# Performance work log

Measured on AMD Instinct MI355X. Metric: run time of the kernel, lower is better.

## Reference

```python
import jax, jax.numpy as jnp
import numpy as np
from jax import lax

EPS = 1e-05


def rmsnorm_axis1(x, w, eps=EPS):
    # RMS over channel axis (axis=1), scale by per-channel weight
    ms = jnp.mean(x * x, axis=1, keepdims=True)
    return x * lax.rsqrt(ms + eps) * w[None, :, None]


def dwconv1d(x, w, b, dilation):
    # x: [B, C, L]; w: [C, 1, K] depthwise (feature_group_count=C)
    pad = (w.shape[-1] - 1) // 2 * dilation
    y = lax.conv_general_dilated(
        x, w, window_strides=(1,), padding=[(pad, pad)],
        rhs_dilation=(dilation,), dimension_numbers=('NCH', 'OIH', 'NCH'),
        feature_group_count=x.shape[1])
    return y + b[None, :, None]


def setup_inputs() -> dict:
    key = jax.random.key(0)
    ks = jax.random.split(key, 12)
    B, C, L, K = 16, 512, 2048, 3
    s = 1.0 / np.sqrt(C)
    return {
        'number_log': jax.random.normal(ks[0], (B,), jnp.float32),
        'x': jax.random.normal(ks[1], (B, C, L), jnp.float32),
        'pre_w': jnp.ones((C,), jnp.float32),
        'conv_w': jax.random.normal(ks[2], (C, 1, K), jnp.float32) * 0.3,
        'conv_b': jnp.zeros((C,), jnp.float32),
        'conv1_w': jax.random.normal(ks[3], (C, 1, K), jnp.float32) * 0.3,
        'conv1_b': jnp.zeros((C,), jnp.float32),
        'conv2_w': jax.random.normal(ks[4], (C, 1, K), jnp.float32) * 0.3,
        'conv2_b': jnp.zeros((C,), jnp.float32),
        'gate_w': jax.random.normal(ks[5], (C, C), jnp.float32) * s,
        'gate_b': jnp.zeros((C,), jnp.float32),
        'post_w': jnp.ones((C,), jnp.float32),
        'logits_w': jax.random.normal(ks[6], (1, C, 1), jnp.float32) * s,
    }


def reference(number_log, x, pre_w, conv_w, conv_b, conv1_w, conv1_b,
              conv2_w, conv2_b, gate_w, gate_b, post_w, logits_w):
    # pre_norm over channel axis
    x_norm = rmsnorm_axis1(x, pre_w)
    # three dilated depthwise conv branches, summed
    x_d = (dwconv1d(x_norm, conv_w, conv_b, 1)
           + dwconv1d(x_norm, conv1_w, conv1_b, 2)
           + dwconv1d(x_norm, conv2_w, conv2_b, 4))
    # gate: Linear over channel dim of transposed input, SiLU
    gate = jax.nn.silu(jnp.einsum('bcl,dc->bdl', x_norm, gate_w)
                       + gate_b[None, :, None])
    x_d = rmsnorm_axis1(x_d * gate, post_w)
    # logits: 1x1 conv C->1, no bias
    out = jnp.einsum('bcl,oc->bol', x + x_d, logits_w[:, :, 0])
    return out
```

## Files before the change

kernel.cpp:

```cpp
#include <hip/hip_runtime.h>
#include <hip/hip_bf16.h>

#define BB 16
#define CC 512
#define LL 2048

typedef float f32x4 __attribute__((ext_vector_type(4)));
typedef short s16x8 __attribute__((ext_vector_type(8)));

static __device__ __forceinline__ float bf2f(unsigned short u) {
    union { unsigned int i; float f; } v; v.i = ((unsigned int)u) << 16; return v.f;
}
static __device__ __forceinline__ unsigned short f2bf(float f) {
    union { float fv; unsigned int i; } v; v.fv = f;
    unsigned int x = v.i;
    return (unsigned short)((x + 0x7FFFu + ((x >> 16) & 1u)) >> 16);
}

__global__ void k0_cast(const float* __restrict__ gw, unsigned short* __restrict__ gwb) {
    int i = blockIdx.x * 256 + threadIdx.x;
    if (i < CC * CC) gwb[i] = f2bf(gw[i]);
}

#define K1_ST 520
__global__ __launch_bounds__(256) void k1_rms_t(
    const float* __restrict__ x, const float* __restrict__ pre_w,
    unsigned short* __restrict__ xnt, float* __restrict__ invr) {
    __shared__ unsigned short tile[32 * K1_ST];
    __shared__ float red[32 * 33];
    __shared__ float pwS[CC];
    __shared__ float ivS[32];
    const int tid = threadIdx.x;
    const int b  = blockIdx.x >> 6;
    const int lt = blockIdx.x & 63;
    const int l0 = lt * 32;
    const float* xb = x + (size_t)(b * CC) * LL + l0;

    for (int i = tid; i < CC; i += 256) pwS[i] = pre_w[i];

    const int lq = tid & 7;
    const int cr = tid >> 3;
    f32x4 ssq = {0.f, 0.f, 0.f, 0.f};
    #pragma unroll
    for (int p = 0; p < 16; ++p) {
        int c = p * 32 + cr;
        f32x4 v = *(const f32x4*)(xb + (size_t)c * LL + lq * 4);
        #pragma unroll
        for (int r = 0; r < 4; ++r) {
            ssq[r] += v[r] * v[r];
            tile[(lq * 4 + r) * K1_ST + c] = f2bf(v[r]);
        }
    }
    #pragma unroll
    for (int r = 0; r < 4; ++r) red[(lq * 4 + r) * 33 + cr] = ssq[r];
    __syncthreads();
    if (tid < 32) {
        float s = 0.f;
        #pragma unroll
        for (int g = 0; g < 32; ++g) s += red[tid * 33 + g];
        float iv = rsqrtf(s * (1.0f / CC) + 1e-5f);
        ivS[tid] = iv;
        invr[b * LL + l0 + tid] = iv;
    }
    __syncthreads();
    unsigned short* xo = xnt + ((size_t)b * LL + l0) * CC;
    #pragma unroll
    for (int p = 0; p < 8; ++p) {
        int g = p * 256 + tid;
        int l = g >> 6, c8 = (g & 63) * 8;
        s16x8 t = *(const s16x8*)&tile[l * K1_ST + c8];
        f32x4 w0 = *(const f32x4*)&pwS[c8];
        f32x4 w1 = *(const f32x4*)&pwS[c8 + 4];
        float iv = ivS[l];
        s16x8 o;
        #pragma unroll
        for (int r = 0; r < 4; ++r) {
            o[r]     = (short)f2bf(bf2f((unsigned short)t[r])     * iv * w0[r]);
            o[r + 4] = (short)f2bf(bf2f((unsigned short)t[r + 4]) * iv * w1[r]);
        }
        *(s16x8*)(xo + (size_t)l * CC + c8) = o;
    }
}

__global__ __launch_bounds__(512, 2) void k2_gemm(
    const unsigned short* __restrict__ gwb,
    const unsigned short* __restrict__ xnt,
    const float* __restrict__ gate_b,
    unsigned short* __restrict__ gate) {
    __shared__ unsigned short As[2][256 * 64];
    __shared__ unsigned short Bs[2][256 * 64];
    const int tid = threadIdx.x;
    const int w = tid >> 6, lane = tid & 63;
    const int lo = lane & 15, hi = lane >> 4;
    const int wm = w >> 2, wn = w & 3;
    const int nt = blockIdx.x, mt = blockIdx.y, b = blockIdx.z;
    const int m0 = mt * 256, n0 = nt * 256;
    const unsigned short* Ab = gwb;
    const unsigned short* Bb = xnt + (size_t)b * LL * CC;

    #define K2_STG(pp, buf, kt_)                                                     \
        {                                                                            \
            int g = (pp) * 512 + tid;                                                \
            int row = g >> 3;                                                        \
            int ks = ((g & 7) * 8) ^ ((row & 4) ? 16 : 0);                           \
            __builtin_amdgcn_global_load_lds(                                        \
                (const __attribute__((address_space(1))) void*)(Ab + (size_t)(m0 + row) * CC + (kt_) * 64 + ks), \
                (__attribute__((address_space(3))) void*)(&As[buf][g * 8]),          \
                16, 0, 0);                                                           \
            __builtin_amdgcn_global_load_lds(                                        \
                (const __attribute__((address_space(1))) void*)(Bb + (size_t)(n0 + row) * CC + (kt_) * 64 + ks), \
                (__attribute__((address_space(3))) void*)(&Bs[buf][g * 8]),          \
                16, 0, 0);                                                           \
        }

    f32x4 acc[8][4] = {};

    #pragma unroll
    for (int p = 0; p < 4; ++p) K2_STG(p, 0, 0);
    asm volatile("s_waitcnt vmcnt(0)" ::: "memory");
    __builtin_amdgcn_s_barrier();

    #pragma unroll 2
    for (int kt = 0; kt < 8; ++kt) {
        const int cur = kt & 1;
        s16x8 bf[4][2];
        #pragma unroll
        for (int p = 0; p < 4; ++p) {
            s16x8 af[2][2];
            #pragma unroll
            for (int j = 0; j < 2; ++j) {
                int row = wm * 128 + (p * 2 + j) * 16 + lo;
                int kb = (row & 4) ? 16 : 0;
                #pragma unroll
                for (int kk = 0; kk < 2; ++kk)
                    af[j][kk] = *(const s16x8*)(&As[cur][row * 64 + ((kk * 32 + hi * 8) ^ kb)]);
            }
            if (p == 0) {
                #pragma unroll
                for (int ni = 0; ni < 4; ++ni) {
                    int row = wn * 64 + ni * 16 + lo;
                    int kb = (row & 4) ? 16 : 0;
                    #pragma unroll
                    for (int kk = 0; kk < 2; ++kk)
                        bf[ni][kk] = *(const s16x8*)(&Bs[cur][row * 64 + ((kk * 32 + hi * 8) ^ kb)]);
                }
            }
            if (kt < 7) K2_STG(p, cur ^ 1, kt + 1);
            __builtin_amdgcn_s_barrier();
            asm volatile("s_waitcnt lgkmcnt(0)" ::: "memory");
            __builtin_amdgcn_sched_barrier(0);
            __builtin_amdgcn_s_setprio(1);
            #pragma unroll
            for (int j = 0; j < 2; ++j)
                #pragma unroll
                for (int ni = 0; ni < 4; ++ni)
                    #pragma unroll
                    for (int kk = 0; kk < 2; ++kk)
                        acc[p * 2 + j][ni] = __builtin_amdgcn_mfma_f32_16x16x32_bf16(
                            af[j][kk], bf[ni][kk], acc[p * 2 + j][ni], 0, 0, 0);
            __builtin_amdgcn_s_setprio(0);
            if (p == 3) asm volatile("s_waitcnt vmcnt(0)" ::: "memory");
            __builtin_amdgcn_s_barrier();
        }
    }

    #pragma unroll
    for (int mi = 0; mi < 8; ++mi) {
        #pragma unroll
        for (int ni = 0; ni < 4; ++ni) {
            int n = n0 + wn * 64 + ni * 16 + lo;
            int d0 = m0 + wm * 128 + mi * 16 + hi * 4;
            #pragma unroll
            for (int r = 0; r < 4; ++r) {
                int d = d0 + r;
                float z = acc[mi][ni][r] + gate_b[d];
                float s = z / (1.0f + __expf(-z));
                gate[((size_t)(b * CC + d)) * LL + n] = f2bf(s);
            }
        }
    }
}

__global__ __launch_bounds__(256) void k3a(
    const float* __restrict__ x, const float* __restrict__ invr,
    const unsigned short* __restrict__ gate,
    const float* __restrict__ cw0, const float* __restrict__ cb0,
    const float* __restrict__ cw1, const float* __restrict__ cb1,
    const float* __restrict__ cw2, const float* __restrict__ cb2,
    const float* __restrict__ pre_w, const float* __restrict__ post_w,
    const float* __restrict__ lw, float* __restrict__ part) {
    __shared__ float tapS[64][8];
    __shared__ float biasS[64], preS[64], lwS[64], pwlwS[64];
    __shared__ float ivs[136];
    __shared__ float red[8][128][3];
    const int tid = threadIdx.x;
    const int lt = blockIdx.x;
    const int cc = blockIdx.y;
    const int b  = blockIdx.z;
    const int l0 = lt * 128;
    const int c0 = cc * 64;

    if (tid < 64) {
        int c = c0 + tid;
        float w10 = cw0[c*3], w11 = cw0[c*3+1], w12 = cw0[c*3+2];
        float w20 = cw1[c*3], w21 = cw1[c*3+1], w22 = cw1[c*3+2];
        float w40 = cw2[c*3], w41 = cw2[c*3+1], w42 = cw2[c*3+2];
        tapS[tid][0] = w40; tapS[tid][1] = w20; tapS[tid][2] = w10;
        tapS[tid][3] = w11 + w21 + w41;
        tapS[tid][4] = w12; tapS[tid][5] = w22; tapS[tid][6] = w42;
        biasS[tid] = cb0[c] + cb1[c] + cb2[c];
        preS[tid]  = pre_w[c];
        float lwc = lw[c];
        lwS[tid] = lwc;
        pwlwS[tid] = post_w[c] * lwc;
    }
    if (tid < 136) {
        int lg = l0 - 4 + tid;
        ivs[tid] = (lg >= 0 && lg < LL) ? invr[b * LL + lg] : 0.f;
    }
    __syncthreads();

    const int li = tid & 31, ci = tid >> 5;
    const int lq = l0 + li * 4;
    float iv[12];
    #pragma unroll
    for (int j = 0; j < 12; ++j) iv[j] = ivs[li * 4 + j];

    const int ia = (lq - 4 < 0) ? 0 : lq - 4;
    const int ic = (lq + 4 > LL - 4) ? LL - 4 : lq + 4;

    float ass[4] = {}, adp[4] = {}, adx[4] = {};
    const float* xbase = x + ((size_t)(b * CC + c0)) * LL;
    const unsigned short* gbase = gate + ((size_t)(b * CC + c0)) * LL;

    #pragma unroll
    for (int j = 0; j < 8; ++j) {
        const int cl = ci * 8 + j;
        const float* xr = xbase + (size_t)cl * LL;
        f32x4 xa = *(const f32x4*)(xr + ia);
        f32x4 xm = *(const f32x4*)(xr + lq);
        f32x4 xc = *(const f32x4*)(xr + ic);
        uint2 gu = *(const uint2*)(gbase + (size_t)cl * LL + lq);
        float g[4];
        g[0] = bf2f((unsigned short)(gu.x & 0xffff));
        g[1] = bf2f((unsigned short)(gu.x >> 16));
        g[2] = bf2f((unsigned short)(gu.y & 0xffff));
        g[3] = bf2f((unsigned short)(gu.y >> 16));
        float z[12];
        #pragma unroll
        for (int r = 0; r < 4; ++r) {
            z[r]     = xa[r] * iv[r];
            z[r + 4] = xm[r] * iv[r + 4];
            z[r + 8] = xc[r] * iv[r + 8];
        }
        const float t0 = tapS[cl][0], t1 = tapS[cl][1], t2 = tapS[cl][2],
                    t3 = tapS[cl][3], t4 = tapS[cl][4], t5 = tapS[cl][5],
                    t6 = tapS[cl][6];
        const float pre = preS[cl], bias = biasS[cl], pwlw = pwlwS[cl], lwc = lwS[cl];
        #pragma unroll
        for (int k = 0; k < 4; ++k) {
            float s = t0 * z[k] + t1 * z[k + 2] + t2 * z[k + 3] + t3 * z[k + 4]
                    + t4 * z[k + 5] + t5 * z[k + 6] + t6 * z[k + 8];
            float p = (pre * s + bias) * g[k];
            ass[k] += p * p;
            adp[k] += p * pwlw;
            adx[k] += xm[k] * lwc;
        }
    }
    #pragma unroll
    for (int k = 0; k < 4; ++k) {
        red[ci][li * 4 + k][0] = ass[k];
        red[ci][li * 4 + k][1] = adp[k];
        red[ci][li * 4 + k][2] = adx[k];
    }
    __syncthreads();
    if (tid < 128) {
        float s0 = 0.f, s1 = 0.f, s2 = 0.f;
        #pragma unroll
        for (int g2 = 0; g2 < 8; ++g2) {
            s0 += red[g2][tid][0];
            s1 += red[g2][tid][1];
            s2 += red[g2][tid][2];
        }
        float* pp = part + (((size_t)(b * 8 + cc)) * LL + l0 + tid) * 3;
        pp[0] = s0; pp[1] = s1; pp[2] = s2;
    }
}

__global__ __launch_bounds__(256) void k3b(
    const float* __restrict__ part, float* __restrict__ out) {
    int gl = blockIdx.x * 256 + threadIdx.x;
    int b = gl >> 11, l = gl & 2047;
    float s0 = 0.f, s1 = 0.f, s2 = 0.f;
    #pragma unroll
    for (int cc2 = 0; cc2 < 8; ++cc2) {
        const float* pp = part + (((size_t)(b * 8 + cc2)) * LL + l) * 3;
        s0 += pp[0]; s1 += pp[1]; s2 += pp[2];
    }
    out[gl] = s2 + rsqrtf(s0 * (1.0f / CC) + 1e-5f) * s1;
}

extern "C" void kernel_launch(void* const* d_in, const int* in_sizes, int n_in,
                              void* d_out, int out_size, void* d_ws, size_t ws_size,
                              hipStream_t stream) {
    const float* x      = (const float*)d_in[1];
    const float* pre_w  = (const float*)d_in[2];
    const float* cw0    = (const float*)d_in[3];
    const float* cb0    = (const float*)d_in[4];
    const float* cw1    = (const float*)d_in[5];
    const float* cb1    = (const float*)d_in[6];
    const float* cw2    = (const float*)d_in[7];
    const float* cb2    = (const float*)d_in[8];
    const float* gw     = (const float*)d_in[9];
    const float* gb     = (const float*)d_in[10];
    const float* post_w = (const float*)d_in[11];
    const float* lw     = (const float*)d_in[12];
    float* out = (float*)d_out;

    char* ws = (char*)d_ws;
    unsigned short* gwb  = (unsigned short*)(ws);
    unsigned short* xnt  = (unsigned short*)(ws + 524288);
    float*          invr = (float*)(ws + 524288 + 33554432);
    unsigned short* gate = (unsigned short*)(ws + 524288 + 33554432 + 131072);
    float*          part = (float*)(ws + 524288);

    hipLaunchKernelGGL(k0_cast,  dim3((CC * CC + 255) / 256), dim3(256), 0, stream, gw, gwb);
    hipLaunchKernelGGL(k1_rms_t, dim3(BB * (LL / 32)),        dim3(256), 0, stream, x, pre_w, xnt, invr);
    hipLaunchKernelGGL(k2_gemm,  dim3(LL / 256, CC / 256, BB), dim3(512), 0, stream, gwb, xnt, gb, gate);
    hipLaunchKernelGGL(k3a,      dim3(LL / 128, CC / 64, BB), dim3(256), 0, stream,
                       x, invr, gate, cw0, cb0, cw1, cb1, cw2, cb2, pre_w, post_w, lw, part);
    hipLaunchKernelGGL(k3b,      dim3(BB * LL / 256),         dim3(256), 0, stream, part, out);
}
```

Measured before the change: 79.16 us.

## Fuse gate GEMM with depthwise conv, post-norm and logits epilogue

The gate GEMM becomes one kernel per (batch, 128-length tile) that computes all 512 output channels, with a triple-buffered K-loop of depth 32. Its epilogue applies SiLU in registers, stages gate tiles and normalized input slices in LDS, evaluates the three dilated convolutions, and reduces the post-RMS and logits terms directly to the output. The x·logits dot product moves into the first pass. This drops the bf16 gate round trip through HBM, the second read of x, and the separate partial-sum and reduce kernels. In exchange the grid shrinks to 256 blocks, and the conv now reads bf16 normalized input instead of fp32 x.

After: 179.1 us. 126% more time.

```diff
diff --git a/kernel.cpp b/kernel.cpp
--- a/kernel.cpp
+++ b/kernel.cpp
@@ -25,10 +25,13 @@
 #define K1_ST 520
 __global__ __launch_bounds__(256) void k1_rms_t(
     const float* __restrict__ x, const float* __restrict__ pre_w,
-    unsigned short* __restrict__ xnt, float* __restrict__ invr) {
+    const float* __restrict__ lw,
+    unsigned short* __restrict__ xnt, float* __restrict__ adx) {
     __shared__ unsigned short tile[32 * K1_ST];
     __shared__ float red[32 * 33];
+    __shared__ float red2[32 * 33];
     __shared__ float pwS[CC];
+    __shared__ float lwS[CC];
     __shared__ float ivS[32];
     const int tid = threadIdx.x;
     const int b  = blockIdx.x >> 6;
@@ -36,31 +39,37 @@
     const int l0 = lt * 32;
     const float* xb = x + (size_t)(b * CC) * LL + l0;
 
-    for (int i = tid; i < CC; i += 256) pwS[i] = pre_w[i];
+    for (int i = tid; i < CC; i += 256) { pwS[i] = pre_w[i]; lwS[i] = lw[i]; }
+    __syncthreads();
 
     const int lq = tid & 7;
     const int cr = tid >> 3;
     f32x4 ssq = {0.f, 0.f, 0.f, 0.f};
+    f32x4 sdx = {0.f, 0.f, 0.f, 0.f};
     #pragma unroll
     for (int p = 0; p < 16; ++p) {
         int c = p * 32 + cr;
+        float lwc = lwS[c];
         f32x4 v = *(const f32x4*)(xb + (size_t)c * LL + lq * 4);
         #pragma unroll
         for (int r = 0; r < 4; ++r) {
             ssq[r] += v[r] * v[r];
+            sdx[r] += v[r] * lwc;
             tile[(lq * 4 + r) * K1_ST + c] = f2bf(v[r]);
         }
     }
     #pragma unroll
-    for (int r = 0; r < 4; ++r) red[(lq * 4 + r) * 33 + cr] = ssq[r];
+    for (int r = 0; r < 4; ++r) {
+        red[(lq * 4 + r) * 33 + cr]  = ssq[r];
+        red2[(lq * 4 + r) * 33 + cr] = sdx[r];
+    }
     __syncthreads();
     if (tid < 32) {
-        float s = 0.f;
-        #pragma unroll
-        for (int g = 0; g < 32; ++g) s += red[tid * 33 + g];
-        float iv = rsqrtf(s * (1.0f / CC) + 1e-5f);
-        ivS[tid] = iv;
-        invr[b * LL + l0 + tid] = iv;
+        float s = 0.f, sa = 0.f;
+        #pragma unroll
+        for (int g = 0; g < 32; ++g) { s += red[tid * 33 + g]; sa += red2[tid * 33 + g]; }
+        ivS[tid] = rsqrtf(s * (1.0f / CC) + 1e-5f);
+        adx[b * LL + l0 + tid] = sa;
     }
     __syncthreads();
     unsigned short* xo = xnt + ((size_t)b * LL + l0) * CC;
@@ -82,222 +91,188 @@
     }
 }
 
-__global__ __launch_bounds__(512, 2) void k2_gemm(
+__global__ __launch_bounds__(512, 2) void k2_fused(
     const unsigned short* __restrict__ gwb,
     const unsigned short* __restrict__ xnt,
     const float* __restrict__ gate_b,
-    unsigned short* __restrict__ gate) {
-    __shared__ unsigned short As[2][256 * 64];
-    __shared__ unsigned short Bs[2][256 * 64];
+    const float* __restrict__ cw0, const float* __restrict__ cb0,
+    const float* __restrict__ cw1, const float* __restrict__ cb1,
+    const float* __restrict__ cw2, const float* __restrict__ cb2,
+    const float* __restrict__ post_w, const float* __restrict__ lw,
+    const float* __restrict__ adx, float* __restrict__ out) {
+    union Sm {
+        struct { unsigned short A[3][512 * 32]; unsigned short B[3][128 * 32]; } g;
+        struct { unsigned short xnc[136 * 128]; unsigned short gS[128 * 128]; } e;
+    };
+    __shared__ Sm sm;
     const int tid = threadIdx.x;
     const int w = tid >> 6, lane = tid & 63;
     const int lo = lane & 15, hi = lane >> 4;
-    const int wm = w >> 2, wn = w & 3;
-    const int nt = blockIdx.x, mt = blockIdx.y, b = blockIdx.z;
-    const int m0 = mt * 256, n0 = nt * 256;
+    const int wm = w >> 1, wn = w & 1;
+    const int lt = blockIdx.x, b = blockIdx.z;
+    const int l0 = lt * 128;
     const unsigned short* Ab = gwb;
     const unsigned short* Bb = xnt + (size_t)b * LL * CC;
 
-    #define K2_STG(pp, buf, kt_)                                                     \
-        {                                                                            \
-            int g = (pp) * 512 + tid;                                                \
-            int row = g >> 3;                                                        \
-            int ks = ((g & 7) * 8) ^ ((row & 4) ? 16 : 0);                           \
-            __builtin_amdgcn_global_load_lds(                                        \
-                (const __attribute__((address_space(1))) void*)(Ab + (size_t)(m0 + row) * CC + (kt_) * 64 + ks), \
-                (__attribute__((address_space(3))) void*)(&As[buf][g * 8]),          \
-                16, 0, 0);                                                           \
-            __builtin_amdgcn_global_load_lds(                                        \
-                (const __attribute__((address_space(1))) void*)(Bb + (size_t)(n0 + row) * CC + (kt_) * 64 + ks), \
-                (__attribute__((address_space(3))) void*)(&Bs[buf][g * 8]),          \
-                16, 0, 0);                                                           \
+    #define STG(kt_, buf_)                                                            \
+        {                                                                             \
+            _Pragma("unroll")                                                         \
+            for (int r_ = 0; r_ < 4; ++r_) {                                          \
+                int row_ = (tid >> 2) + r_ * 128, gin_ = tid & 3;                     \
+                __builtin_amdgcn_global_load_lds(                                     \
+                    (const __attribute__((address_space(1))) void*)(Ab + (size_t)row_ * CC + (kt_) * 32 + ((gin_ ^ ((row_ >> 1) & 3)) * 8)), \
+                    (__attribute__((address_space(3))) void*)(&sm.g.A[buf_][(row_ * 32 + gin_ * 8)]), \
+                    16, 0, 0);                                                        \
+            }                                                                         \
+            {                                                                         \
+                int row_ = tid >> 2, gin_ = tid & 3;                                  \
+                __builtin_amdgcn_global_load_lds(                                     \
+                    (const __attribute__((address_space(1))) void*)(Bb + (size_t)(l0 + row_) * CC + (kt_) * 32 + ((gin_ ^ ((row_ >> 1) & 3)) * 8)), \
+                    (__attribute__((address_space(3))) void*)(&sm.g.B[buf_][tid * 8]), \
+                    16, 0, 0);                                                        \
+            }                                                                         \
         }
 
     f32x4 acc[8][4] = {};
-
-    #pragma unroll
-    for (int p = 0; p < 4; ++p) K2_STG(p, 0, 0);
-    asm volatile("s_waitcnt vmcnt(0)" ::: "memory");
-    __builtin_amdgcn_s_barrier();
-
-    #pragma unroll 2
-    for (int kt = 0; kt < 8; ++kt) {
-        const int cur = kt & 1;
-        s16x8 bf[4][2];
-        #pragma unroll
-        for (int p = 0; p < 4; ++p) {
-            s16x8 af[2][2];
+    const int fsw = (lo >> 1) & 3;
+
+    STG(0, 0);
+    STG(1, 1);
+    #pragma unroll
+    for (int kt = 0; kt < 16; ++kt) {
+        const int buf = kt % 3;
+        if (kt < 14) STG(kt + 2, (kt + 2) % 3);
+        if (kt < 14)      asm volatile("s_waitcnt vmcnt(10)" ::: "memory");
+        else if (kt == 14) asm volatile("s_waitcnt vmcnt(5)" ::: "memory");
+        else               asm volatile("s_waitcnt vmcnt(0)" ::: "memory");
+        __builtin_amdgcn_s_barrier();
+        s16x8 af[8], bfr[4];
+        #pragma unroll
+        for (int mi = 0; mi < 8; ++mi)
+            af[mi] = *(const s16x8*)&sm.g.A[buf][(wm * 128 + mi * 16 + lo) * 32 + ((hi ^ fsw) * 8)];
+        #pragma unroll
+        for (int ni = 0; ni < 4; ++ni)
+            bfr[ni] = *(const s16x8*)&sm.g.B[buf][(wn * 64 + ni * 16 + lo) * 32 + ((hi ^ fsw) * 8)];
+        __builtin_amdgcn_s_setprio(1);
+        #pragma unroll
+        for (int mi = 0; mi < 8; ++mi)
             #pragma unroll
-            for (int j = 0; j < 2; ++j) {
-                int row = wm * 128 + (p * 2 + j) * 16 + lo;
-                int kb = (row & 4) ? 16 : 0;
-                #pragma unroll
-                for (int kk = 0; kk < 2; ++kk)
-                    af[j][kk] = *(const s16x8*)(&As[cur][row * 64 + ((kk * 32 + hi * 8) ^ kb)]);
+            for (int ni = 0; ni < 4; ++ni)
+                acc[mi][ni] = __builtin_amdgcn_mfma_f32_16x16x32_bf16(
+                    af[mi], bfr[ni], acc[mi][ni], 0, 0, 0);
+        __builtin_amdgcn_s_setprio(0);
+        asm volatile("" ::: "memory");
+        __builtin_amdgcn_s_barrier();
+    }
+    #undef STG
+
+    unsigned int gpk[8][4][2];
+    #pragma unroll
+    for (int mi = 0; mi < 8; ++mi) {
+        f32x4 gb4 = *(const f32x4*)(gate_b + wm * 128 + mi * 16 + hi * 4);
+        #pragma unroll
+        for (int ni = 0; ni < 4; ++ni) {
+            f32x4 z = acc[mi][ni] + gb4;
+            float s0 = z[0] / (1.0f + __expf(-z[0]));
+            float s1 = z[1] / (1.0f + __expf(-z[1]));
+            float s2 = z[2] / (1.0f + __expf(-z[2]));
+            float s3 = z[3] / (1.0f + __expf(-z[3]));
+            gpk[mi][ni][0] = (unsigned int)f2bf(s0) | ((unsigned int)f2bf(s1) << 16);
+            gpk[mi][ni][1] = (unsigned int)f2bf(s2) | ((unsigned int)f2bf(s3) << 16);
+        }
+    }
+
+    float pass[4] = {}, padp[4] = {};
+    const int cg = tid & 15, o = tid >> 4;
+    #pragma unroll
+    for (int q = 0; q < 4; ++q) {
+        #pragma unroll
+        for (int r = 0; r < 5; ++r) {
+            int gi = tid + r * 512;
+            if (gi < 2176) {
+                int row = gi >> 4, gin = gi & 15;
+                int lg = l0 - 4 + row;
+                lg = lg < 0 ? 0 : (lg > LL - 1 ? LL - 1 : lg);
+                __builtin_amdgcn_global_load_lds(
+                    (const __attribute__((address_space(1))) void*)(Bb + (size_t)lg * CC + q * 128 + ((gin ^ (row & 7)) * 8)),
+                    (__attribute__((address_space(3))) void*)(&sm.e.xnc[gi * 8]),
+                    16, 0, 0);
             }
-            if (p == 0) {
+        }
+        asm volatile("s_waitcnt vmcnt(0)" ::: "memory");
+        __builtin_amdgcn_s_barrier();
+        if (l0 == 0 && tid < 64) {
+            s16x8 z8 = {};
+            *(s16x8*)&sm.e.xnc[(tid >> 4) * 128 + (tid & 15) * 8] = z8;
+        }
+        if (l0 == LL - 128 && tid < 64) {
+            s16x8 z8 = {};
+            *(s16x8*)&sm.e.xnc[(132 + (tid >> 4)) * 128 + (tid & 15) * 8] = z8;
+        }
+        if (wm == q) {
+            #pragma unroll
+            for (int mi = 0; mi < 8; ++mi)
                 #pragma unroll
                 for (int ni = 0; ni < 4; ++ni) {
-                    int row = wn * 64 + ni * 16 + lo;
-                    int kb = (row & 4) ? 16 : 0;
-                    #pragma unroll
-                    for (int kk = 0; kk < 2; ++kk)
-                        bf[ni][kk] = *(const s16x8*)(&Bs[cur][row * 64 + ((kk * 32 + hi * 8) ^ kb)]);
+                    int lg = wn * 64 + ni * 16 + lo;
+                    int coff = (mi * 16 + hi * 4) ^ ((lg & 7) << 3);
+                    *(uint2*)&sm.e.gS[lg * 128 + coff] = make_uint2(gpk[mi][ni][0], gpk[mi][ni][1]);
                 }
+        }
+        __builtin_amdgcn_s_barrier();
+        s16x8 xr[12];
+        #pragma unroll
+        for (int t = 0; t < 12; ++t) {
+            int row = o * 4 + t;
+            xr[t] = *(const s16x8*)&sm.e.xnc[row * 128 + ((cg ^ (row & 7)) * 8)];
+        }
+        s16x8 gr[4];
+        #pragma unroll
+        for (int i = 0; i < 4; ++i) {
+            int lg = o * 4 + i;
+            gr[i] = *(const s16x8*)&sm.e.gS[lg * 128 + ((cg * 8) ^ ((lg & 7) << 3))];
+        }
+        #pragma unroll
+        for (int j = 0; j < 8; ++j) {
+            int c = q * 128 + cg * 8 + j;
+            float t10 = cw0[c * 3], t11 = cw0[c * 3 + 1], t12 = cw0[c * 3 + 2];
+            float t20 = cw1[c * 3], t21 = cw1[c * 3 + 1], t22 = cw1[c * 3 + 2];
+            float t40 = cw2[c * 3], t41 = cw2[c * 3 + 1], t42 = cw2[c * 3 + 2];
+            float bias = cb0[c] + cb1[c] + cb2[c];
+            float tc = t11 + t21 + t41;
+            float pwlw = post_w[c] * lw[c];
+            float xf[12];
+            #pragma unroll
+            for (int t = 0; t < 12; ++t) xf[t] = bf2f((unsigned short)xr[t][j]);
+            #pragma unroll
+            for (int i = 0; i < 4; ++i) {
+                float s = t40 * xf[i] + t20 * xf[i + 2] + t10 * xf[i + 3]
+                        + tc * xf[i + 4] + t12 * xf[i + 5] + t22 * xf[i + 6]
+                        + t42 * xf[i + 8];
+                float p = (s + bias) * bf2f((unsigned short)gr[i][j]);
+                pass[i] += p * p;
+                padp[i] += p * pwlw;
             }
-            if (kt < 7) K2_STG(p, cur ^ 1, kt + 1);
-            __builtin_amdgcn_s_barrier();
-            asm volatile("s_waitcnt lgkmcnt(0)" ::: "memory");
-            __builtin_amdgcn_sched_barrier(0);
-            __builtin_amdgcn_s_setprio(1);
-            #pragma unroll
-            for (int j = 0; j < 2; ++j)
-                #pragma unroll
-                for (int ni = 0; ni < 4; ++ni)
-                    #pragma unroll
-                    for (int kk = 0; kk < 2; ++kk)
-                        acc[p * 2 + j][ni] = __builtin_amdgcn_mfma_f32_16x16x32_bf16(
-                            af[j][kk], bf[ni][kk], acc[p * 2 + j][ni], 0, 0, 0);
-            __builtin_amdgcn_s_setprio(0);
-            if (p == 3) asm volatile("s_waitcnt vmcnt(0)" ::: "memory");
-            __builtin_amdgcn_s_barrier();
-        }
-    }
-
-    #pragma unroll
-    for (int mi = 0; mi < 8; ++mi) {
-        #pragma unroll
-        for (int ni = 0; ni < 4; ++ni) {
-            int n = n0 + wn * 64 + ni * 16 + lo;
-            int d0 = m0 + wm * 128 + mi * 16 + hi * 4;
-            #pragma unroll
-            for (int r = 0; r < 4; ++r) {
-                int d = d0 + r;
-                float z = acc[mi][ni][r] + gate_b[d];
-                float s = z / (1.0f + __expf(-z));
-                gate[((size_t)(b * CC + d)) * LL + n] = f2bf(s);
-            }
-        }
-    }
-}
-
-__global__ __launch_bounds__(256) void k3a(
-    const float* __restrict__ x, const float* __restrict__ invr,
-    const unsigned short* __restrict__ gate,
-    const float* __restrict__ cw0, const float* __restrict__ cb0,
-    const float* __restrict__ cw1, const float* __restrict__ cb1,
-    const float* __restrict__ cw2, const float* __restrict__ cb2,
-    const float* __restrict__ pre_w, const float* __restrict__ post_w,
-    const float* __restrict__ lw, float* __restrict__ part) {
-    __shared__ float tapS[64][8];
-    __shared__ float biasS[64], preS[64], lwS[64], pwlwS[64];
-    __shared__ float ivs[136];
-    __shared__ float red[8][128][3];
-    const int tid = threadIdx.x;
-    const int lt = blockIdx.x;
-    const int cc = blockIdx.y;
-    const int b  = blockIdx.z;
-    const int l0 = lt * 128;
-    const int c0 = cc * 64;
-
-    if (tid < 64) {
-        int c = c0 + tid;
-        float w10 = cw0[c*3], w11 = cw0[c*3+1], w12 = cw0[c*3+2];
-        float w20 = cw1[c*3], w21 = cw1[c*3+1], w22 = cw1[c*3+2];
-        float w40 = cw2[c*3], w41 = cw2[c*3+1], w42 = cw2[c*3+2];
-        tapS[tid][0] = w40; tapS[tid][1] = w20; tapS[tid][2] = w10;
-        tapS[tid][3] = w11 + w21 + w41;
-        tapS[tid][4] = w12; tapS[tid][5] = w22; tapS[tid][6] = w42;
-        biasS[tid] = cb0[c] + cb1[c] + cb2[c];
-        preS[tid]  = pre_w[c];
-        float lwc = lw[c];
-        lwS[tid] = lwc;
-        pwlwS[tid] = post_w[c] * lwc;
-    }
-    if (tid < 136) {
-        int lg = l0 - 4 + tid;
-        ivs[tid] = (lg >= 0 && lg < LL) ? invr[b * LL + lg] : 0.f;
-    }
-    __syncthreads();
-
-    const int li = tid & 31, ci = tid >> 5;
-    const int lq = l0 + li * 4;
-    float iv[12];
-    #pragma unroll
-    for (int j = 0; j < 12; ++j) iv[j] = ivs[li * 4 + j];
-
-    const int ia = (lq - 4 < 0) ? 0 : lq - 4;
-    const int ic = (lq + 4 > LL - 4) ? LL - 4 : lq + 4;
-
-    float ass[4] = {}, adp[4] = {}, adx[4] = {};
-    const float* xbase = x + ((size_t)(b * CC + c0)) * LL;
-    const unsigned short* gbase = gate + ((size_t)(b * CC + c0)) * LL;
-
-    #pragma unroll
-    for (int j = 0; j < 8; ++j) {
-        const int cl = ci * 8 + j;
-        const float* xr = xbase + (size_t)cl * LL;
-        f32x4 xa = *(const f32x4*)(xr + ia);
-        f32x4 xm = *(const f32x4*)(xr + lq);
-        f32x4 xc = *(const f32x4*)(xr + ic);
-        uint2 gu = *(const uint2*)(gbase + (size_t)cl * LL + lq);
-        float g[4];
-        g[0] = bf2f((unsigned short)(gu.x & 0xffff));
-        g[1] = bf2f((unsigned short)(gu.x >> 16));
-        g[2] = bf2f((unsigned short)(gu.y & 0xffff));
-        g[3] = bf2f((unsigned short)(gu.y >> 16));
-        float z[12];
-        #pragma unroll
-        for (int r = 0; r < 4; ++r) {
-            z[r]     = xa[r] * iv[r];
-            z[r + 4] = xm[r] * iv[r + 4];
-            z[r + 8] = xc[r] * iv[r + 8];
-        }
-        const float t0 = tapS[cl][0], t1 = tapS[cl][1], t2 = tapS[cl][2],
-                    t3 = tapS[cl][3], t4 = tapS[cl][4], t5 = tapS[cl][5],
-                    t6 = tapS[cl][6];
-        const float pre = preS[cl], bias = biasS[cl], pwlw = pwlwS[cl], lwc = lwS[cl];
-        #pragma unroll
-        for (int k = 0; k < 4; ++k) {
-            float s = t0 * z[k] + t1 * z[k + 2] + t2 * z[k + 3] + t3 * z[k + 4]
-                    + t4 * z[k + 5] + t5 * z[k + 6] + t6 * z[k + 8];
-            float p = (pre * s + bias) * g[k];
-            ass[k] += p * p;
-            adp[k] += p * pwlw;
-            adx[k] += xm[k] * lwc;
-        }
-    }
-    #pragma unroll
-    for (int k = 0; k < 4; ++k) {
-        red[ci][li * 4 + k][0] = ass[k];
-        red[ci][li * 4 + k][1] = adp[k];
-        red[ci][li * 4 + k][2] = adx[k];
-    }
-    __syncthreads();
-    if (tid < 128) {
-        float s0 = 0.f, s1 = 0.f, s2 = 0.f;
-        #pragma unroll
-        for (int g2 = 0; g2 < 8; ++g2) {
-            s0 += red[g2][tid][0];
-            s1 += red[g2][tid][1];
-            s2 += red[g2][tid][2];
-        }
-        float* pp = part + (((size_t)(b * 8 + cc)) * LL + l0 + tid) * 3;
-        pp[0] = s0; pp[1] = s1; pp[2] = s2;
-    }
-}
-
-__global__ __launch_bounds__(256) void k3b(
-    const float* __restrict__ part, float* __restrict__ out) {
-    int gl = blockIdx.x * 256 + threadIdx.x;
-    int b = gl >> 11, l = gl & 2047;
-    float s0 = 0.f, s1 = 0.f, s2 = 0.f;
-    #pragma unroll
-    for (int cc2 = 0; cc2 < 8; ++cc2) {
-        const float* pp = part + (((size_t)(b * 8 + cc2)) * LL + l) * 3;
-        s0 += pp[0]; s1 += pp[1]; s2 += pp[2];
-    }
-    out[gl] = s2 + rsqrtf(s0 * (1.0f / CC) + 1e-5f) * s1;
+        }
+        asm volatile("" ::: "memory");
+        __builtin_amdgcn_s_barrier();
+    }
+    #pragma unroll
+    for (int m = 1; m < 16; m <<= 1) {
+        #pragma unroll
+        for (int i = 0; i < 4; ++i) {
+            pass[i] += __shfl_xor(pass[i], m, 64);
+            padp[i] += __shfl_xor(padp[i], m, 64);
+        }
+    }
+    if (cg == 0) {
+        #pragma unroll
+        for (int i = 0; i < 4; ++i) {
+            int lg = l0 + o * 4 + i;
+            out[(size_t)b * LL + lg] = adx[b * LL + lg]
+                + rsqrtf(pass[i] * (1.0f / CC) + 1e-5f) * padp[i];
+        }
+    }
 }
 
 extern "C" void kernel_launch(void* const* d_in, const int* in_sizes, int n_in,
@@ -318,16 +293,13 @@
     float* out = (float*)d_out;
 
     char* ws = (char*)d_ws;
-    unsigned short* gwb  = (unsigned short*)(ws);
-    unsigned short* xnt  = (unsigned short*)(ws + 524288);
-    float*          invr = (float*)(ws + 524288 + 33554432);
-    unsigned short* gate = (unsigned short*)(ws + 524288 + 33554432 + 131072);
-    float*          part = (float*)(ws + 524288);
+    unsigned short* gwb = (unsigned short*)(ws);
+    unsigned short* xnt = (unsigned short*)(ws + 524288);
+    float*          adx = (float*)(ws + 524288 + 33554432);
 
     hipLaunchKernelGGL(k0_cast,  dim3((CC * CC + 255) / 256), dim3(256), 0, stream, gw, gwb);
-    hipLaunchKernelGGL(k1_rms_t, dim3(BB * (LL / 32)),        dim3(256), 0, stream, x, pre_w, xnt, invr);
-    hipLaunchKernelGGL(k2_gemm,  dim3(LL / 256, CC / 256, BB), dim3(512), 0, stream, gwb, xnt, gb, gate);
-    hipLaunchKernelGGL(k3a,      dim3(LL / 128, CC / 64, BB), dim3(256), 0, stream,
-                       x, invr, gate, cw0, cb0, cw1, cb1, cw2, cb2, pre_w, post_w, lw, part);
-    hipLaunchKernelGGL(k3b,      dim3(BB * LL / 256),         dim3(256), 0, stream, part, out);
-}
+    hipLaunchKernelGGL(k1_rms_t, dim3(BB * (LL / 32)),        dim3(256), 0, stream,
+                       x, pre_w, lw, xnt, adx);
+    hipLaunchKernelGGL(k2_fused, dim3(LL / 128, 1, BB),       dim3(512), 0, stream,
+                       gwb, xnt, gb, cw0, cb0, cw1, cb1, cw2, cb2, post_w, lw, adx, out);
+}
```

## Restructure gate GEMM into triple-buffered K=32 pipeline with two-stage prefetch

Applied to the files above, without the earlier changes.

The gate GEMM's LDS staging changes from a double buffer of K=64 tiles, loaded in four sub-phases, to a triple buffer of K=32 tiles with loads issued two iterations ahead and partial vmcnt waits. The swizzle is reworked for the narrower 32-element rows. The goal is to keep more global loads in flight and hide load latency behind the MFMA work. The cost is one barrier pair per 32-wide K step, twice as many as before, and fewer MFMAs between barriers.

Result: no change. 78.64 us (-0.7%).

```diff
diff --git a/kernel.cpp b/kernel.cpp
--- a/kernel.cpp
+++ b/kernel.cpp
@@ -87,8 +87,8 @@
     const unsigned short* __restrict__ xnt,
     const float* __restrict__ gate_b,
     unsigned short* __restrict__ gate) {
-    __shared__ unsigned short As[2][256 * 64];
-    __shared__ unsigned short Bs[2][256 * 64];
+    __shared__ unsigned short As[3][256 * 32];
+    __shared__ unsigned short Bs[3][256 * 32];
     const int tid = threadIdx.x;
     const int w = tid >> 6, lane = tid & 63;
     const int lo = lane & 15, hi = lane >> 4;
@@ -98,71 +98,60 @@
     const unsigned short* Ab = gwb;
     const unsigned short* Bb = xnt + (size_t)b * LL * CC;
 
-    #define K2_STG(pp, buf, kt_)                                                     \
-        {                                                                            \
-            int g = (pp) * 512 + tid;                                                \
-            int row = g >> 3;                                                        \
-            int ks = ((g & 7) * 8) ^ ((row & 4) ? 16 : 0);                           \
-            __builtin_amdgcn_global_load_lds(                                        \
-                (const __attribute__((address_space(1))) void*)(Ab + (size_t)(m0 + row) * CC + (kt_) * 64 + ks), \
-                (__attribute__((address_space(3))) void*)(&As[buf][g * 8]),          \
-                16, 0, 0);                                                           \
-            __builtin_amdgcn_global_load_lds(                                        \
-                (const __attribute__((address_space(1))) void*)(Bb + (size_t)(n0 + row) * CC + (kt_) * 64 + ks), \
-                (__attribute__((address_space(3))) void*)(&Bs[buf][g * 8]),          \
-                16, 0, 0);                                                           \
+    #define STG(kt_, buf_)                                                            \
+        {                                                                             \
+            _Pragma("unroll")                                                         \
+            for (int s_ = 0; s_ < 2; ++s_) {                                          \
+                int g_ = tid + s_ * 512;                                              \
+                int row_ = g_ >> 2, gin_ = g_ & 3;                                    \
+                int ks_ = (kt_) * 32 + ((gin_ ^ ((row_ >> 1) & 3)) * 8);              \
+                __builtin_amdgcn_global_load_lds(                                     \
+                    (const __attribute__((address_space(1))) void*)(Ab + (size_t)(m0 + row_) * CC + ks_), \
+                    (__attribute__((address_space(3))) void*)(&As[buf_][g_ * 8]),     \
+                    16, 0, 0);                                                        \
+                __builtin_amdgcn_global_load_lds(                                     \
+                    (const __attribute__((address_space(1))) void*)(Bb + (size_t)(n0 + row_) * CC + ks_), \
+                    (__attribute__((address_space(3))) void*)(&Bs[buf_][g_ * 8]),     \
+                    16, 0, 0);                                                        \
+            }                                                                         \
         }
 
     f32x4 acc[8][4] = {};
-
-    #pragma unroll
-    for (int p = 0; p < 4; ++p) K2_STG(p, 0, 0);
-    asm volatile("s_waitcnt vmcnt(0)" ::: "memory");
-    __builtin_amdgcn_s_barrier();
-
-    #pragma unroll 2
-    for (int kt = 0; kt < 8; ++kt) {
-        const int cur = kt & 1;
-        s16x8 bf[4][2];
-        #pragma unroll
-        for (int p = 0; p < 4; ++p) {
-            s16x8 af[2][2];
+    const int fsw = (lo >> 1) & 3;
+
+    STG(0, 0);
+    STG(1, 1);
+    #pragma unroll
+    for (int kt = 0; kt < 16; ++kt) {
+        const int buf = kt % 3;
+        if (kt < 14) {
+            STG(kt + 2, (kt + 2) % 3);
+            asm volatile("s_waitcnt vmcnt(8)" ::: "memory");
+        } else if (kt == 14) {
+            asm volatile("s_waitcnt vmcnt(4)" ::: "memory");
+        } else {
+            asm volatile("s_waitcnt vmcnt(0)" ::: "memory");
+        }
+        __builtin_amdgcn_s_barrier();
+        s16x8 af[8], bfr[4];
+        #pragma unroll
+        for (int mi = 0; mi < 8; ++mi)
+            af[mi] = *(const s16x8*)&As[buf][(wm * 128 + mi * 16 + lo) * 32 + ((hi ^ fsw) * 8)];
+        #pragma unroll
+        for (int ni = 0; ni < 4; ++ni)
+            bfr[ni] = *(const s16x8*)&Bs[buf][(wn * 64 + ni * 16 + lo) * 32 + ((hi ^ fsw) * 8)];
+        __builtin_amdgcn_s_setprio(1);
+        #pragma unroll
+        for (int mi = 0; mi < 8; ++mi)
             #pragma unroll
-            for (int j = 0; j < 2; ++j) {
-                int row = wm * 128 + (p * 2 + j) * 16 + lo;
-                int kb = (row & 4) ? 16 : 0;
-                #pragma unroll
-                for (int kk = 0; kk < 2; ++kk)
-                    af[j][kk] = *(const s16x8*)(&As[cur][row * 64 + ((kk * 32 + hi * 8) ^ kb)]);
-            }
-            if (p == 0) {
-                #pragma unroll
-                for (int ni = 0; ni < 4; ++ni) {
-                    int row = wn * 64 + ni * 16 + lo;
-                    int kb = (row & 4) ? 16 : 0;
-                    #pragma unroll
-                    for (int kk = 0; kk < 2; ++kk)
-                        bf[ni][kk] = *(const s16x8*)(&Bs[cur][row * 64 + ((kk * 32 + hi * 8) ^ kb)]);
-                }
-            }
-            if (kt < 7) K2_STG(p, cur ^ 1, kt + 1);
-            __builtin_amdgcn_s_barrier();
-            asm volatile("s_waitcnt lgkmcnt(0)" ::: "memory");
-            __builtin_amdgcn_sched_barrier(0);
-            __builtin_amdgcn_s_setprio(1);
-            #pragma unroll
-            for (int j = 0; j < 2; ++j)
-                #pragma unroll
-                for (int ni = 0; ni < 4; ++ni)
-                    #pragma unroll
-                    for (int kk = 0; kk < 2; ++kk)
-                        acc[p * 2 + j][ni] = __builtin_amdgcn_mfma_f32_16x16x32_bf16(
-                            af[j][kk], bf[ni][kk], acc[p * 2 + j][ni], 0, 0, 0);
-            __builtin_amdgcn_s_setprio(0);
-            if (p == 3) asm volatile("s_waitcnt vmcnt(0)" ::: "memory");
-            __builtin_amdgcn_s_barrier();
-        }
-    }
+            for (int ni = 0; ni < 4; ++ni)
+                acc[mi][ni] = __builtin_amdgcn_mfma_f32_16x16x32_bf16(
+                    af[mi], bfr[ni], acc[mi][ni], 0, 0, 0);
+        __builtin_amdgcn_s_setprio(0);
+        asm volatile("" ::: "memory");
+        __builtin_amdgcn_s_barrier();
+    }
+    #undef STG
 
     #pragma unroll
     for (int mi = 0; mi < 8; ++mi) {
```
